# Kernel optimization log

Hardware: AMD Instinct MI355X
Metric: run time of the kernel (lower is better)

## Reference

```python
import jax, jax.numpy as jnp
import numpy as np

FIXED_DELTA_LAMBDA = 0.04226162119141463


def setup_inputs() -> dict:
    key = jax.random.key(0)
    B, H, W, S = 4, 512, 512, 128
    L_hr = jax.random.normal(key, (B, H, W, S), dtype=jnp.float32)
    # HyPlant FLUO-like spectral grid: 670-780 nm
    sensor_wavelengths = jnp.linspace(670.0, 780.0, S, dtype=jnp.float32)
    return {
        "L_hr": L_hr,
        "delta_lambda": jnp.float32(0.0),
        "delta_sigma": jnp.float32(0.0),
        "sensor_wavelengths": sensor_wavelengths,
    }


def reference(L_hr, delta_lambda, delta_sigma, sensor_wavelengths):
    # L_hr: [B, H, W, spec]; output: [B, spec, H, W]
    n = sensor_wavelengths.shape[0]
    wl_min = sensor_wavelengths.min()
    wl_max = sensor_wavelengths.max()
    high_res = (wl_max - wl_min) / n  # matches (max-min)/len in __init__
    # lambda_hr = linspace(wl_min, wl_max, n) with traced endpoints
    lambda_hr = wl_min + (wl_max - wl_min) * jnp.arange(n, dtype=L_hr.dtype) / (n - 1)

    sigma = (0.27 + delta_sigma) * 2.3548
    # NOTE: the torch module also computes a Gaussian conv1d blur (L_blur) that is
    # never used in the output (dead code); we faithfully reproduce the output math.
    # delta_lambda is also unused: the module applies fixed_delta_lambda instead.
    effective_wl = sensor_wavelengths + FIXED_DELTA_LAMBDA  # [spec]
    diff = lambda_hr[None, :] - effective_wl[:, None]       # [spec, spec]
    g = jnp.exp(-0.5 * (diff / sigma) ** 2)
    g = g / (g.sum(axis=1, keepdims=True) + 1e-6)
    # 'ij,bjhw->bihw' after permute(0,3,1,2) == 'ij,bhwj->bihw' on the raw layout
    return jnp.einsum("ij,bhwj->bihw", g, L_hr) * high_res
```

## Files before the change

kernel.cpp:

```cpp
#include <hip/hip_runtime.h>
#include <hip/hip_bf16.h>


#define S_CH   128
#define HW_PLN (512 * 512)
#define TPX    64
#define RS     137
#define NTAP   9
#define RADIUS 4

__global__ void hyplant_taps_kernel(const float* __restrict__ sw,
                                    const float* __restrict__ dsig,
                                    float* __restrict__ w_out) {
    const int i = threadIdx.x;
    const int n = S_CH;
    float wl_min = sw[0], wl_max = sw[0];
    for (int j = 1; j < n; ++j) {
        float v = sw[j];
        wl_min = fminf(wl_min, v);
        wl_max = fmaxf(wl_max, v);
    }
    const float span     = wl_max - wl_min;
    const float high_res = span / (float)n;
    const float sigma    = (0.27f + dsig[0]) * 2.3548f;
    const float inv_s    = 1.0f / sigma;
    const float ewl      = sw[i] + 0.04226162119141463f;

    float sum = 0.0f;
    for (int j = 0; j < n; ++j) {
        float lhr = wl_min + (span * (float)j) / 127.0f;
        float d   = (lhr - ewl) * inv_s;
        sum += expf(-0.5f * d * d);
    }
    const float scale = high_res / (sum + 1e-6f);

    for (int t = 0; t < NTAP; ++t) {
        int   j = i - RADIUS + t;
        float w = 0.0f;
        if (j >= 0 && j < n) {
            float lhr = wl_min + (span * (float)j) / 127.0f;
            float d   = (lhr - ewl) * inv_s;
            w = expf(-0.5f * d * d) * scale;
        }
        w_out[i * NTAP + t] = w;
    }
}

__global__ __launch_bounds__(256) void hyplant_sim_kernel(
        const float* __restrict__ L,
        const float* __restrict__ w_g,
        float* __restrict__ out) {
    __shared__ float lds[TPX * RS];
    __shared__ float wl[S_CH * NTAP];

    const int bid = blockIdx.x;
    const int b   = bid >> 12;
    const int hw0 = (bid & 4095) << 6;
    const int tid = threadIdx.x;

    for (int idx = tid; idx < S_CH * NTAP; idx += 256) wl[idx] = w_g[idx];

    for (int idx = tid; idx < TPX * 8; idx += 256) {
        int row = idx >> 3, q = idx & 7;
        lds[row * RS + (q < 4 ? q : 128 + q)] = 0.0f;
    }

    const float4* src = (const float4*)(L + ((size_t)b * HW_PLN + hw0) * S_CH);
    for (int idx = tid; idx < TPX * 32; idx += 256) {
        int    p  = idx >> 5, f4 = idx & 31;
        float4 v  = src[p * 32 + f4];
        int    ba = p * RS + RADIUS + f4 * 4;
        lds[ba]     = v.x;
        lds[ba + 1] = v.y;
        lds[ba + 2] = v.z;
        lds[ba + 3] = v.w;
    }
    __syncthreads();

    const int p = tid & 63;
    const int c = (tid >> 6) << 5;

    float r[32 + 2 * RADIUS];
    const int rb = p * RS + c;
#pragma unroll
    for (int k = 0; k < 32 + 2 * RADIUS; ++k) r[k] = lds[rb + k];

    float* outp = out + ((size_t)(b * S_CH + c)) * HW_PLN + hw0 + p;
#pragma unroll
    for (int il = 0; il < 32; ++il) {
        float acc = 0.0f;
#pragma unroll
        for (int t = 0; t < NTAP; ++t)
            acc = fmaf(wl[(c + il) * NTAP + t], r[il + t], acc);
        outp[(size_t)il * HW_PLN] = acc;
    }
}

extern "C" void kernel_launch(void* const* d_in, const int* in_sizes, int n_in,
                              void* d_out, int out_size, void* d_ws, size_t ws_size,
                              hipStream_t stream) {
    const float* L    = (const float*)d_in[0];
    const float* dsig = (const float*)d_in[2];
    const float* sw   = (const float*)d_in[3];
    float*       out  = (float*)d_out;
    float*       taps = (float*)d_ws;

    hyplant_taps_kernel<<<1, 128, 0, stream>>>(sw, dsig, taps);

    const int total_pixels = in_sizes[0] / S_CH;
    const int grid         = total_pixels / TPX;
    hyplant_sim_kernel<<<grid, 256, 0, stream>>>(L, taps, out);
}
```

Before: 226.6 us.

## Load spectra directly into registers, drop LDS staging, use nontemporal stores

Each thread now reads its own pixel's 40-channel window (including halo) straight from global memory into registers as float4s, removing the LDS staging buffer, its zero-fill and the block barrier. Tap weights come from global memory through a wave-uniform pointer instead of an LDS copy, and the channel-group index is made wave-uniform with readfirstlane so those loads can be scalar. Output writes become nontemporal stores to avoid polluting the cache. The cost is that each thread issues strided 512-byte-apart float4 loads, so global coalescing is worse and halo channels are read twice across the four channel groups.

```diff
diff --git a/kernel.cpp b/kernel.cpp
--- a/kernel.cpp
+++ b/kernel.cpp
@@ -4,8 +4,6 @@
 
 #define S_CH   128
 #define HW_PLN (512 * 512)
-#define TPX    64
-#define RS     137
 #define NTAP   9
 #define RADIUS 4
 
@@ -50,40 +48,45 @@
         const float* __restrict__ L,
         const float* __restrict__ w_g,
         float* __restrict__ out) {
-    __shared__ float lds[TPX * RS];
-    __shared__ float wl[S_CH * NTAP];
-
+    const int tid = threadIdx.x;
     const int bid = blockIdx.x;
     const int b   = bid >> 12;
     const int hw0 = (bid & 4095) << 6;
-    const int tid = threadIdx.x;
+    const int p   = tid & 63;
+    const int c   = __builtin_amdgcn_readfirstlane((tid >> 6) << 5);
 
-    for (int idx = tid; idx < S_CH * NTAP; idx += 256) wl[idx] = w_g[idx];
+    const float4* row = (const float4*)(L + ((size_t)b * HW_PLN + hw0 + p) * S_CH);
+    float r[32 + 2 * RADIUS];
 
-    for (int idx = tid; idx < TPX * 8; idx += 256) {
-        int row = idx >> 3, q = idx & 7;
-        lds[row * RS + (q < 4 ? q : 128 + q)] = 0.0f;
+    if (c == 0) {
+#pragma unroll
+        for (int k = 0; k < 4; ++k) r[k] = 0.0f;
+#pragma unroll
+        for (int q = 0; q < 9; ++q) {
+            float4 v = row[q];
+            r[4 + 4 * q] = v.x; r[5 + 4 * q] = v.y;
+            r[6 + 4 * q] = v.z; r[7 + 4 * q] = v.w;
+        }
+    } else if (c == 96) {
+#pragma unroll
+        for (int q = 0; q < 9; ++q) {
+            float4 v = row[23 + q];
+            r[4 * q]     = v.x; r[4 * q + 1] = v.y;
+            r[4 * q + 2] = v.z; r[4 * q + 3] = v.w;
+        }
+#pragma unroll
+        for (int k = 36; k < 40; ++k) r[k] = 0.0f;
+    } else {
+        const int i0 = (c >> 2) - 1;
+#pragma unroll
+        for (int q = 0; q < 10; ++q) {
+            float4 v = row[i0 + q];
+            r[4 * q]     = v.x; r[4 * q + 1] = v.y;
+            r[4 * q + 2] = v.z; r[4 * q + 3] = v.w;
+        }
     }
 
-    const float4* src = (const float4*)(L + ((size_t)b * HW_PLN + hw0) * S_CH);
-    for (int idx = tid; idx < TPX * 32; idx += 256) {
-        int    p  = idx >> 5, f4 = idx & 31;
-        float4 v  = src[p * 32 + f4];
-        int    ba = p * RS + RADIUS + f4 * 4;
-        lds[ba]     = v.x;
-        lds[ba + 1] = v.y;
-        lds[ba + 2] = v.z;
-        lds[ba + 3] = v.w;
-    }
-    __syncthreads();
-
-    const int p = tid & 63;
-    const int c = (tid >> 6) << 5;
-
-    float r[32 + 2 * RADIUS];
-    const int rb = p * RS + c;
-#pragma unroll
-    for (int k = 0; k < 32 + 2 * RADIUS; ++k) r[k] = lds[rb + k];
+    const float* __restrict__ wg = w_g + c * NTAP;
 
     float* outp = out + ((size_t)(b * S_CH + c)) * HW_PLN + hw0 + p;
 #pragma unroll
@@ -91,8 +94,8 @@
         float acc = 0.0f;
 #pragma unroll
         for (int t = 0; t < NTAP; ++t)
-            acc = fmaf(wl[(c + il) * NTAP + t], r[il + t], acc);
-        outp[(size_t)il * HW_PLN] = acc;
+            acc = fmaf(wg[il * NTAP + t], r[il + t], acc);
+        __builtin_nontemporal_store(acc, outp + (size_t)il * HW_PLN);
     }
 }
 
@@ -108,6 +111,6 @@
     hyplant_taps_kernel<<<1, 128, 0, stream>>>(sw, dsig, taps);
 
     const int total_pixels = in_sizes[0] / S_CH;
-    const int grid         = total_pixels / TPX;
+    const int grid         = total_pixels / 64;
     hyplant_sim_kernel<<<grid, 256, 0, stream>>>(L, taps, out);
 }
```

Measured after the change: 341.2 us. +50.6%, slower.
